# Optimization experiments

Hardware: AMD Instinct MI355X
Metric: run time of the kernel (lower is better)

## Reference

```python
import jax, jax.numpy as jnp
import numpy as np

B, N, R, S, FIN, NCLS, KNN = 16, 2048, 64, 64, 6, 40, 40


def _knn_laplacian(x, k):
    # pairwise squared distance -> gaussian affinity -> row-wise top-k sparsify
    # -> symmetric-normalized Laplacian  L = I - D^{-1/2} A D^{-1/2}
    xx = jnp.sum(x * x, axis=-1)                      # [B,N]
    inner = jnp.einsum('bnd,bmd->bnm', x, x)          # [B,N,N]
    dist = xx[:, :, None] + xx[:, None, :] - 2.0 * inner
    A = jnp.exp(-dist)
    kth = jax.lax.top_k(A, k)[0][..., -1]             # k-th largest per row [B,N]
    A = jnp.where(A >= kth[..., None], A, jnp.zeros((), A.dtype))
    d = jnp.sum(A, axis=-1)
    dis = jnp.where(d > 0, jax.lax.rsqrt(jnp.maximum(d, 1e-12)), jnp.zeros((), A.dtype))
    L = jnp.eye(A.shape[-1], dtype=A.dtype) - dis[:, :, None] * A * dis[:, None, :]
    return L


def _cheb_conv(x, L, w, b):
    # DenseChebConv, K=3: T0=x, T1=Lx, T2=2LT1-T0, then linear on concat
    t0 = x
    t1 = jnp.matmul(L, x)
    t2 = 2.0 * jnp.matmul(L, t1) - t0
    xc = jnp.concatenate([t0, t1, t2], axis=-1)       # [B,N,3*Fin]
    return jnp.matmul(xc, w) + b


def setup_inputs() -> dict:
    key = jax.random.key(0)
    ks = jax.random.split(key, 16)
    p = lambda k_, sh: (jax.random.normal(k_, sh, dtype=jnp.float32) * 0.02)
    return {
        'x': jax.random.normal(ks[0], (B, N, FIN), dtype=jnp.float32),
        'laplacian_Reeb': jax.random.normal(ks[1], (B, R, R), dtype=jnp.float32),
        'sccs': jax.random.randint(ks[2], (B, R, S), 0, N),
        'vertices_reeb': jax.random.normal(ks[3], (B * R, 3), dtype=jnp.float32),
        'edges_reeb': jax.random.randint(ks[4], (B, 128, 2), 0, R),
        'labels': jax.random.randint(ks[5], (B,), 0, NCLS),
        'k': KNN, 'batch_size': B, 'num_points': N,
        'conv1_w': p(ks[6], (3 * FIN, 128)), 'conv1_b': jnp.zeros((128,), jnp.float32),
        'conv2_w': p(ks[7], (3 * 128, 512)), 'conv2_b': jnp.zeros((512,), jnp.float32),
        'convReeb_w': p(ks[8], (3 * 128, 512)), 'convReeb_b': jnp.zeros((512,), jnp.float32),
        'fc1_w': p(ks[9], (1024, 512)), 'fc1_b': jnp.zeros((512,), jnp.float32),
        'fc2_w': p(ks[10], (512, 128)), 'fc2_b': jnp.zeros((128,), jnp.float32),
        'fc3_w': p(ks[11], (128, NCLS)), 'fc3_b': jnp.zeros((NCLS,), jnp.float32),
    }


def reference(x, laplacian_Reeb, sccs, vertices_reeb, edges_reeb, labels, k,
              batch_size, num_points, conv1_w, conv1_b, conv2_w, conv2_b,
              convReeb_w, convReeb_b, fc1_w, fc1_b, fc2_w, fc2_b, fc3_w, fc3_b):
    regs = []
    # graph build is under no_grad in the original
    L = jax.lax.stop_gradient(_knn_laplacian(x, k))
    out = jax.nn.relu(_cheb_conv(x, L, conv1_w, conv1_b))           # [B,N,128]
    regs.append(jnp.linalg.norm(jnp.einsum('bnf,bnm,bmg->bfg', out, L, out)) ** 2)

    # Reeb ragged segment-max pool (no_grad in original): gather SCC index
    # groups per Reeb node and max-reduce -> [B,R,128]
    gathered = jax.vmap(lambda o, s: o[s])(out, sccs)               # [B,R,S,128]
    Vertices_final_Reeb = jax.lax.stop_gradient(jnp.max(gathered, axis=2))
    laplacian_Reeb_final = jax.lax.stop_gradient(laplacian_Reeb)

    L2 = jax.lax.stop_gradient(_knn_laplacian(out, k))
    out = jax.nn.relu(_cheb_conv(out, L2, conv2_w, conv2_b))        # [B,N,512]
    regs.append(jnp.linalg.norm(jnp.einsum('bnf,bnm,bmg->bfg', out, L2, out)) ** 2)

    out_Reeb = jax.nn.relu(_cheb_conv(Vertices_final_Reeb, laplacian_Reeb_final,
                                      convReeb_w, convReeb_b))      # [B,R,512]
    regs.append(jnp.linalg.norm(jnp.einsum('brf,brq,bqg->bfg', out_Reeb,
                                           laplacian_Reeb_final, out_Reeb)) ** 2)

    out = jnp.max(out, axis=1)            # [B,512]
    out_Reeb = jnp.max(out_Reeb, axis=1)  # [B,512]
    out = jnp.concatenate([out_Reeb, out], axis=1)                  # [B,1024]

    out = jnp.matmul(out, fc1_w) + fc1_b
    regs.append(jnp.linalg.norm(fc1_w[:, 0]) ** 2); regs.append(fc1_b[0] ** 2)
    out = jax.nn.relu(out)
    out = jnp.matmul(out, fc2_w) + fc2_b
    regs.append(jnp.linalg.norm(fc2_w[:, 0]) ** 2); regs.append(fc2_b[0] ** 2)
    out = jax.nn.relu(out)
    out = jnp.matmul(out, fc3_w) + fc3_b
    regs.append(jnp.linalg.norm(fc3_w[:, 0]) ** 2); regs.append(fc3_b[0] ** 2)
    return out, jnp.stack(regs)
```

## Files before the change

kernel.cpp:

```cpp
#include <hip/hip_runtime.h>

#define NB 16
#define NP 2048
#define NR 64
#define NS 64
#define KSEL 40

typedef __attribute__((ext_vector_type(8))) short bf16x8;
typedef __attribute__((ext_vector_type(4))) float f32x4;

constexpr long aOUT1 = 0;
constexpr long aT1A  = aOUT1 + 16L*2048*128;
constexpr long aT2A  = aT1A  + 16L*2048*6;
constexpr long aZ1   = aT2A  + 16L*2048*6;
constexpr long aM1   = aZ1   + 16L*2048*128;
constexpr long aVALS1= aM1   + 16L*128*128;
constexpr long aDIS1 = aVALS1+ 16L*2048*64;
constexpr long aVALS2= aDIS1 + 16L*2048;
constexpr long aDIS2 = aVALS2+ 16L*2048*64;
constexpr long aXX2  = aDIS2 + 16L*2048;
constexpr long aXX1  = aXX2  + 16L*2048;
constexpr long aG4   = aXX1  + 16L*2048;
constexpr long aT1B  = aG4   + 4L*2048*2048;
constexpr long aT2B  = aT1B  + 16L*2048*128;
constexpr long aOUT2 = aT2B  + 16L*2048*128;
constexpr long aZ2   = aOUT2 + 16L*2048*512;
constexpr long aVFR  = aZ2   + 16L*2048*512;
constexpr long aT1R  = aVFR  + 16L*64*128;
constexpr long aT2R  = aT1R  + 16L*64*128;
constexpr long aOUTR = aT2R  + 16L*64*128;
constexpr long aZR   = aOUTR + 16L*64*512;
constexpr long aPOOL = aZR   + 16L*64*512;
constexpr long aFC1O = aPOOL + 16L*1024;
constexpr long aFC2O = aFC1O + 16L*512;
constexpr long aMPP  = aFC2O + 16L*128;
constexpr long FTOT  = aMPP  + 16L*8*512;

constexpr long iCOLS1 = 0;
constexpr long iCNT1  = iCOLS1 + 16L*2048*64;
constexpr long iCOLS2 = iCNT1  + 16L*2048;
constexpr long iCNT2  = iCOLS2 + 16L*2048*64;
constexpr long ITOT   = iCNT2  + 16L*2048;

constexpr long uOUT1H = 0;
constexpr long uOUT1L = uOUT1H + 16L*2048*128;
constexpr long uOUT1R = uOUT1L + 16L*2048*128;
constexpr long uT1BH  = uOUT1R + 16L*2048*128;
constexpr long uT1BL  = uT1BH  + 16L*2048*128;
constexpr long uT2BH  = uT1BL  + 16L*2048*128;
constexpr long uT2BL  = uT2BH  + 16L*2048*128;
constexpr long uW2TH  = uT2BL  + 16L*2048*128;
constexpr long uW2TL  = uW2TH  + 512L*384;
constexpr long uVFRH  = uW2TL  + 512L*384;
constexpr long uVFRL  = uVFRH  + 16L*64*128;
constexpr long uT1RH  = uVFRL  + 16L*64*128;
constexpr long uT1RL  = uT1RH  + 16L*64*128;
constexpr long uT2RH  = uT1RL  + 16L*64*128;
constexpr long uT2RL  = uT2RH  + 16L*64*128;
constexpr long uWRTH  = uT2RL  + 16L*64*128;
constexpr long uWRTL  = uWRTH  + 512L*384;
constexpr long uOUT1T = uWRTL  + 512L*384;
constexpr long uZ1T   = uOUT1T + 16L*128*2048;
constexpr long uOUT2T = uZ1T   + 16L*128*2048;
constexpr long uZ2T   = uOUT2T + 16L*512*2048;
constexpr long uOUTRT = uZ2T   + 16L*512*2048;
constexpr long uZRT   = uOUTRT + 16L*512*64;
constexpr long uOUT2B = uZRT   + 16L*512*64;
constexpr long UTOT   = uOUT2B + 16L*2048*512;

__device__ __align__(256) float  g_farena[FTOT];
__device__ __align__(256) int    g_iarena[ITOT];
__device__ __align__(256) ushort g_uarena[UTOT];

__device__ __forceinline__ float wsum_f(float v){
  #pragma unroll
  for (int s=32;s>0;s>>=1) v += __shfl_xor(v, s, 64);
  return v;
}
__device__ __forceinline__ int wsum_i(int v){
  #pragma unroll
  for (int s=32;s>0;s>>=1) v += __shfl_xor(v, s, 64);
  return v;
}

__device__ __forceinline__ void gl2lds16(const void* g, void* l){
  __builtin_amdgcn_global_load_lds(
      (const __attribute__((address_space(1))) void*)g,
      (__attribute__((address_space(3))) void*)l, 16, 0, 0);
}

__device__ __forceinline__ ushort bf_rne(float x){
  unsigned u = __float_as_uint(x);
  u += 0x7fffu + ((u >> 16) & 1u);
  return (ushort)(u >> 16);
}
__device__ __forceinline__ void bf_hilo(float x, ushort& h, ushort& l){
  unsigned u = __float_as_uint(x);
  h = (ushort)(u >> 16);
  float hf = __uint_as_float(u & 0xffff0000u);
  l = (ushort)(__float_as_uint(x - hf) >> 16);
}

__device__ __forceinline__ unsigned fkey(float f){
  unsigned b = __float_as_uint(f);
  return b ^ (((unsigned)((int)b >> 31)) | 0x80000000u);
}
__device__ __forceinline__ float fkey_inv(unsigned k){
  unsigned m = ((unsigned)((int)(~k) >> 31)) | 0x80000000u;
  return __uint_as_float(k ^ m);
}

__device__ __forceinline__ void topk_store(unsigned (&uk)[32], int lane, long row,
    int* __restrict__ cols, float* __restrict__ vals,
    int* __restrict__ cnt, float* __restrict__ dis)
{
  unsigned kmax = uk[0], kmin = uk[0];
  #pragma unroll
  for (int q=1;q<32;++q){
    kmax = kmax > uk[q] ? kmax : uk[q];
    kmin = kmin < uk[q] ? kmin : uk[q];
  }
  #pragma unroll
  for (int s=32;s>0;s>>=1){
    unsigned o1 = (unsigned)__shfl_xor((int)kmax, s, 64);
    unsigned o2 = (unsigned)__shfl_xor((int)kmin, s, 64);
    kmax = kmax > o1 ? kmax : o1;
    kmin = kmin < o2 ? kmin : o2;
  }
  unsigned lo = kmin, hi = kmax + 1u;
  int cLo = 2048, cHi = 0, it = 0;
  while (cLo != KSEL && hi - lo > 1u){
    unsigned t;
    if (it & 1){
      t = lo + ((hi - lo) >> 1);
    } else {
      float flo = fkey_inv(lo), fhi = fkey_inv(hi);
      float ft = flo + (fhi - flo) * ((float)(cLo - KSEL) / (float)(cLo - cHi));
      t = fkey(ft);
      if (t <= lo) t = lo + 1u;
      else if (t >= hi) t = hi - 1u;
    }
    ++it;
    int c = 0;
    #pragma unroll
    for (int q=0;q<32;++q) c += (int)__popcll(__ballot(uk[q] >= t));
    if (c >= KSEL){ lo = t; cLo = c; } else { hi = t; cHi = c; }
  }
  unsigned kth = lo;
  int kc = 0;
  #pragma unroll
  for (int q=0;q<32;++q) kc += (uk[q] >= kth) ? 1 : 0;
  int tot = wsum_i(kc);
  int incl = kc;
  #pragma unroll
  for (int s=1;s<64;s<<=1){ int u = __shfl_up(incl, s, 64); if (lane >= s) incl += u; }
  int pos = incl - kc;
  int* cp = cols + row*64; float* vp = vals + row*64;
  float d = 0.f;
  #pragma unroll
  for (int q=0;q<32;++q){
    if (uk[q] >= kth){
      float v = __expf(fkey_inv(uk[q]));
      d += v;
      if (pos < 64){ cp[pos] = q*64 + lane; vp[pos] = v; }
      pos++;
    }
  }
  d = wsum_f(d);
  if (lane == 0){
    cnt[row] = tot <= 64 ? tot : 64;
    dis[row] = d > 0.f ? (1.0f / sqrtf(fmaxf(d, 1e-12f))) : 0.f;
  }
}

__global__ __launch_bounds__(256) void xx6_kernel(const float* __restrict__ x,
    float* __restrict__ xx1)
{
  long i = (long)blockIdx.x*256 + threadIdx.x;
  const float* p = x + i*6;
  float2 v0 = *(const float2*)(p);
  float2 v1 = *(const float2*)(p+2);
  float2 v2 = *(const float2*)(p+4);
  xx1[i] = v0.x*v0.x + v0.y*v0.y + v1.x*v1.x + v1.y*v1.y + v2.x*v2.x + v2.y*v2.y;
}

__global__ __launch_bounds__(256) void knn1_kernel(const float* __restrict__ x,
    const float* __restrict__ xx1,
    int* __restrict__ cols, float* __restrict__ vals, int* __restrict__ cnt,
    float* __restrict__ dis)
{
  int lane = threadIdx.x & 63;
  long row = (long)blockIdx.x*4 + (threadIdx.x >> 6);
  int b = (int)(row >> 11); int i = (int)(row & (NP-1));
  const float* xb = x + (long)b*NP*6;
  const float* xxb = xx1 + ((long)b << 11);
  float xi[6];
  #pragma unroll
  for (int d2=0; d2<6; ++d2) xi[d2] = xb[(long)i*6 + d2];
  float xxi = xxb[i];
  unsigned uk[32];
  #pragma unroll 4
  for (int c=0;c<32;++c){
    int j = c*64 + lane;
    const float* xj = xb + (long)j*6;
    float2 v0 = *(const float2*)(xj);
    float2 v1 = *(const float2*)(xj+2);
    float2 v2 = *(const float2*)(xj+4);
    float inr = xi[0]*v0.x + xi[1]*v0.y + xi[2]*v1.x + xi[3]*v1.y + xi[4]*v2.x + xi[5]*v2.y;
    uk[c] = fkey(2.f*inr - xxi - xxb[j]);
  }
  topk_store(uk, lane, row, cols, vals, cnt, dis);
}

__global__ __launch_bounds__(256) void knn2_kernel(const float* __restrict__ G,
    const float* __restrict__ xx, int batch0,
    int* __restrict__ cols, float* __restrict__ vals, int* __restrict__ cnt,
    float* __restrict__ dis)
{
  int lane = threadIdx.x & 63;
  long lrow = (long)blockIdx.x*4 + (threadIdx.x >> 6);
  int lb = (int)(lrow >> 11); int i = (int)(lrow & (NP-1));
  long row = ((long)(batch0+lb) << 11) + i;
  const float* Gr = G + ((long)lb*NP + i)*NP;
  const float* xxb = xx + ((long)(batch0+lb) << 11);
  float xxi = xxb[i];
  unsigned uk[32];
  #pragma unroll 4
  for (int c=0;c<32;++c){
    int j = c*64 + lane;
    uk[c] = fkey(2.f*Gr[j] - xxi - xxb[j]);
  }
  topk_store(uk, lane, row, cols, vals, cnt, dis);
}

__global__ __launch_bounds__(256) void spmm6_kernel(const float* __restrict__ X,
    const float* __restrict__ T0, float* __restrict__ Y,
    const int* __restrict__ cols, const float* __restrict__ vals,
    const int* __restrict__ cnt, const float* __restrict__ dis,
    float c1, float c2, float cs)
{
  long row = (long)blockIdx.x*256 + threadIdx.x;
  int b = (int)(row >> 11);
  const float* Xb = X + ((long)b << 11)*6;
  const float* db = dis + ((long)b << 11);
  float acc[6] = {0,0,0,0,0,0};
  int c = cnt[row];
  const int* cp = cols + row*64; const float* vp = vals + row*64;
  for (int t=0;t<c;++t){
    int j = cp[t];
    float w = vp[t] * db[j];
    const float* xr = Xb + (long)j*6;
    #pragma unroll
    for (int d2=0; d2<6; ++d2) acc[d2] += w * xr[d2];
  }
  float di = dis[row];
  #pragma unroll
  for (int d2=0; d2<6; ++d2)
    Y[row*6+d2] = c1*X[row*6+d2] + c2*T0[row*6+d2] - cs*di*acc[d2];
}

template<int W, bool PACK>
__global__ __launch_bounds__((W >= 256) ? 256 : W) void spmm_kernel(
    const float* __restrict__ X, const float* __restrict__ T0, float* __restrict__ Y,
    ushort* __restrict__ Hh, ushort* __restrict__ Ll,
    const int* __restrict__ cols, const float* __restrict__ vals,
    const int* __restrict__ cnt, const float* __restrict__ dis,
    float c1, float c2, float cs)
{
  constexpr int TPB = (W >= 256) ? 256 : W;
  constexpr int E = W / TPB;
  __shared__ int scol[64];
  __shared__ float sval[64];
  int q = blockIdx.x;
  long row = ((long)(q & 7) << 12) + (q >> 3);
  int b = (int)(row >> 11);
  int tid = threadIdx.x;
  int c = cnt[row];
  if (tid < 64){ scol[tid] = cols[row*64+tid]; sval[tid] = vals[row*64+tid]; }
  __syncthreads();
  const float* Xb = X + ((long)b << 11)*W;
  const float* db = dis + ((long)b << 11);
  float acc[E] = {};
  for (int t=0;t<c;++t){
    int j = scol[t];
    float w = sval[t] * db[j];
    const float* xr = Xb + (long)j*W;
    #pragma unroll
    for (int e=0;e<E;++e) acc[e] += w * xr[tid + e*TPB];
  }
  float di = dis[row];
  #pragma unroll
  for (int e=0;e<E;++e){
    long idx = row*W + tid + e*TPB;
    float y = c1*X[idx] + c2*T0[idx] - cs*di*acc[e];
    Y[idx] = y;
    if (PACK){
      ushort h, l; bf_hilo(y, h, l);
      Hh[idx] = h; Ll[idx] = l;
    }
  }
}

__global__ __launch_bounds__(256) void spmmb_kernel(
    const float* __restrict__ X, const ushort* __restrict__ Xb,
    float* __restrict__ Y,
    const int* __restrict__ cols, const float* __restrict__ vals,
    const int* __restrict__ cnt, const float* __restrict__ dis)
{
  __shared__ int scol[4][64];
  __shared__ float sval[4][64];
  int q = blockIdx.x;
  int wid = threadIdx.x >> 6, lane = threadIdx.x & 63;
  long row = ((long)(q & 7) << 12) + ((long)(q >> 3) << 2) + wid;
  int b = (int)(row >> 11);
  scol[wid][lane] = cols[row*64 + lane];
  sval[wid][lane] = vals[row*64 + lane];
  const ushort* Xbb = Xb + ((long)b << 11)*512;
  const float* db = dis + ((long)b << 11);
  int c = cnt[row];
  float acc[8] = {};
  for (int t=0;t<c;++t){
    int j = scol[wid][t];
    float w = sval[wid][t] * db[j];
    bf16x8 v = *(const bf16x8*)(Xbb + (long)j*512 + lane*8);
    #pragma unroll
    for (int e=0;e<8;++e)
      acc[e] += w * __uint_as_float(((unsigned)(ushort)v[e]) << 16);
  }
  float di = dis[row];
  long base = row*512 + lane*8;
  float4 x0 = *(const float4*)(X + base);
  float4 x1 = *(const float4*)(X + base + 4);
  float4 o0, o1;
  o0.x = x0.x - di*acc[0]; o0.y = x0.y - di*acc[1];
  o0.z = x0.z - di*acc[2]; o0.w = x0.w - di*acc[3];
  o1.x = x1.x - di*acc[4]; o1.y = x1.y - di*acc[5];
  o1.z = x1.z - di*acc[6]; o1.w = x1.w - di*acc[7];
  *(float4*)(Y + base) = o0;
  *(float4*)(Y + base + 4) = o1;
}

__global__ __launch_bounds__(128) void conv1_kernel(const float* __restrict__ x,
    const float* __restrict__ t1, const float* __restrict__ t2,
    const float* __restrict__ w, const float* __restrict__ bias,
    float* __restrict__ out, ushort* __restrict__ oh, ushort* __restrict__ ol,
    ushort* __restrict__ orr)
{
  long row = blockIdx.x; int o = threadIdx.x;
  float acc = bias[o];
  const float* xr = x + row*6; const float* a1 = t1 + row*6; const float* a2 = t2 + row*6;
  #pragma unroll
  for (int d2=0; d2<6; ++d2){
    acc += xr[d2]*w[d2*128 + o];
    acc += a1[d2]*w[(6+d2)*128 + o];
    acc += a2[d2]*w[(12+d2)*128 + o];
  }
  acc = fmaxf(acc, 0.f);
  long idx = row*128 + o;
  out[idx] = acc;
  ushort h, l; bf_hilo(acc, h, l);
  oh[idx] = h; ol[idx] = l;
  orr[idx] = bf_rne(acc);
}

template<bool HILO>
__global__ __launch_bounds__(256) void tpack_kernel(const float* __restrict__ X,
    ushort* __restrict__ H, ushort* __restrict__ L,
    int R, int C, long sIn, long sOut)
{
  __shared__ float tile[32][33];
  int c0 = blockIdx.x*32, r0 = blockIdx.y*32, b = blockIdx.z;
  const float* Xb = X + (long)b*sIn;
  int tx = threadIdx.x & 31, ty = threadIdx.x >> 5;
  #pragma unroll
  for (int rr=ty; rr<32; rr+=8)
    tile[rr][tx] = Xb[(long)(r0+rr)*C + c0+tx];
  __syncthreads();
  #pragma unroll
  for (int cc=ty; cc<32; cc+=8){
    float xv = tile[tx][cc];
    long oidx = (long)b*sOut + (long)(c0+cc)*R + r0 + tx;
    if (HILO){
      ushort h, l; bf_hilo(xv, h, l);
      H[oidx] = h; L[oidx] = l;
    } else {
      H[oidx] = bf_rne(xv);
    }
  }
}

template<bool SPLIT, bool CHEB, bool BR, bool TRI>
__global__ __launch_bounds__(256) void mgemm_kernel(
    const ushort* __restrict__ Ah0, const ushort* __restrict__ Ah1, const ushort* __restrict__ Ah2,
    const ushort* __restrict__ Al0, const ushort* __restrict__ Al1, const ushort* __restrict__ Al2,
    const ushort* __restrict__ Bh, const ushort* __restrict__ Bl,
    const float* __restrict__ bias, float* __restrict__ C,
    ushort* __restrict__ Cb, float* __restrict__ ssq,
    int M, int N, int K, long sA, long sB, long sC)
{
  __shared__ ushort AsH[128*32];
  __shared__ ushort BsH[128*32];
  __shared__ ushort AsL[SPLIT ? 128*32 : 8];
  __shared__ ushort BsL[SPLIT ? 128*32 : 8];
  int bz = blockIdx.z;
  int m0, n0;
  if constexpr (TRI){
    int t = blockIdx.x, bx = 0, rem = 16;
    while (t >= rem){ t -= rem; --rem; ++bx; }
    m0 = bx*128; n0 = (bx + t)*128;
  } else {
    m0 = blockIdx.x*128; n0 = blockIdx.y*128;
  }
  int tid = threadIdx.x, lane = tid & 63, wid = tid >> 6;
  int wm = (wid & 1)*64, wn = (wid >> 1)*64;
  f32x4 acc[4][4] = {};
  const ushort* Bb  = Bh + (long)bz*sB;
  const ushort* Blb = SPLIT ? (Bl + (long)bz*sB) : (const ushort*)nullptr;
  const ushort* Ab  = CHEB ? Ah0 : (Ah0 + (long)bz*sA);
  const ushort* Alb = (SPLIT && !CHEB) ? (Al0 + (long)bz*sA) : Al0;

  for (int k0 = 0; k0 < K; k0 += 32){
    #pragma unroll
    for (int cc2=0; cc2<2; ++cc2){
      int chunk = wid*2 + cc2;
      int e = chunk*512 + lane*8;
      int row = e >> 5;
      int slot = (e >> 3) & 3;
      int scol = (slot ^ ((row >> 1) & 3)) * 8;
      const ushort* asrc;
      if (CHEB){
        int kg2 = k0 + scol;
        const ushort* base = (kg2 < 128) ? Ah0 : ((kg2 < 256) ? Ah1 : Ah2);
        asrc = base + (long)(m0+row)*128 + (kg2 & 127);
      } else {
        asrc = Ab + (long)(m0+row)*K + k0 + scol;
      }
      gl2lds16(asrc, &AsH[chunk*512]);
      gl2lds16(Bb + (long)(n0+row)*K + k0 + scol, &BsH[chunk*512]);
      if (SPLIT){
        const ushort* alsrc;
        if (CHEB){
          int kg2 = k0 + scol;
          const ushort* base = (kg2 < 128) ? Al0 : ((kg2 < 256) ? Al1 : Al2);
          alsrc = base + (long)(m0+row)*128 + (kg2 & 127);
        } else {
          alsrc = Alb + (long)(m0+row)*K + k0 + scol;
        }
        gl2lds16(alsrc, &AsL[chunk*512]);
        gl2lds16(Blb + (long)(n0+row)*K + k0 + scol, &BsL[chunk*512]);
      }
    }
    __syncthreads();
    int lr = lane & 15, kg = lane >> 4;
    bf16x8 af[4], bfr[4];
    #pragma unroll
    for (int f=0; f<4; ++f){
      int ra = wm + f*16 + lr;
      int rb = wn + f*16 + lr;
      af[f]  = *(const bf16x8*)&AsH[ra*32 + (kg ^ ((ra>>1)&3))*8];
      bfr[f] = *(const bf16x8*)&BsH[rb*32 + (kg ^ ((rb>>1)&3))*8];
    }
    if (SPLIT){
      bf16x8 al[4], bl[4];
      #pragma unroll
      for (int f=0; f<4; ++f){
        int ra = wm + f*16 + lr;
        int rb = wn + f*16 + lr;
        al[f] = *(const bf16x8*)&AsL[ra*32 + (kg ^ ((ra>>1)&3))*8];
        bl[f] = *(const bf16x8*)&BsL[rb*32 + (kg ^ ((rb>>1)&3))*8];
      }
      #pragma unroll
      for (int mf=0; mf<4; ++mf)
        #pragma unroll
        for (int nf=0; nf<4; ++nf){
          acc[mf][nf] = __builtin_amdgcn_mfma_f32_16x16x32_bf16(af[mf], bfr[nf], acc[mf][nf], 0,0,0);
          acc[mf][nf] = __builtin_amdgcn_mfma_f32_16x16x32_bf16(af[mf], bl[nf],  acc[mf][nf], 0,0,0);
          acc[mf][nf] = __builtin_amdgcn_mfma_f32_16x16x32_bf16(al[mf], bfr[nf], acc[mf][nf], 0,0,0);
        }
    } else {
      #pragma unroll
      for (int mf=0; mf<4; ++mf)
        #pragma unroll
        for (int nf=0; nf<4; ++nf)
          acc[mf][nf] = __builtin_amdgcn_mfma_f32_16x16x32_bf16(af[mf], bfr[nf], acc[mf][nf], 0,0,0);
    }
    __syncthreads();
  }
  int lr = lane & 15, l4 = (lane >> 4)*4;
  if (ssq){
    float s = 0.f;
    #pragma unroll
    for (int mf=0; mf<4; ++mf)
      #pragma unroll
      for (int nf=0; nf<4; ++nf)
        #pragma unroll
        for (int r=0; r<4; ++r){ float v = acc[mf][nf][r]; s += v*v; }
    s = wsum_f(s);
    if (lane == 0) atomicAdd(ssq, s);
    return;
  }
  #pragma unroll
  for (int mf=0; mf<4; ++mf){
    #pragma unroll
    for (int nf=0; nf<4; ++nf){
      int n = n0 + wn + nf*16 + lr;
      float bv = BR ? bias[n] : 0.f;
      #pragma unroll
      for (int r=0; r<4; ++r){
        int m = m0 + wm + mf*16 + l4 + r;
        float v = acc[mf][nf][r];
        if (BR) v = fmaxf(v + bv, 0.f);
        C[(long)bz*sC + (long)m*N + n] = v;
        if (TRI) C[(long)bz*sC + (long)n*N + m] = v;
        if (Cb) Cb[(long)bz*sC + (long)m*N + n] = bf_rne(v);
      }
    }
  }
}

__global__ __launch_bounds__(256) void rownorm_kernel(const float* __restrict__ X,
    float* __restrict__ xx)
{
  int lane = threadIdx.x & 63;
  long row = (long)blockIdx.x*4 + (threadIdx.x >> 6);
  const float* p = X + row*128;
  float v0 = p[lane], v1 = p[64+lane];
  float s = wsum_f(v0*v0 + v1*v1);
  if (lane == 0) xx[row] = s;
}

__global__ __launch_bounds__(128) void reeb_pool_kernel(const float* __restrict__ out1,
    const int* __restrict__ sccs, float* __restrict__ VfR,
    ushort* __restrict__ Hh, ushort* __restrict__ Ll)
{
  int q = blockIdx.x;
  int br = ((q & 7) << 7) + (q >> 3);
  int b = br >> 6;
  int f = threadIdx.x;
  const int* sp = sccs + (long)br*NS;
  const float* ob = out1 + ((long)b << 11)*128;
  float m = -1e30f;
  for (int s=0;s<NS;++s){
    int idx = sp[s];
    m = fmaxf(m, ob[(long)idx*128 + f]);
  }
  long oidx = (long)br*128 + f;
  VfR[oidx] = m;
  ushort h, l; bf_hilo(m, h, l);
  Hh[oidx] = h; Ll[oidx] = l;
}

template<int W, bool PACK>
__global__ __launch_bounds__((W>=256)?256:W) void reeb_mm_kernel(const float* __restrict__ Lap,
    const float* __restrict__ X, const float* __restrict__ T0, float* __restrict__ Y,
    ushort* __restrict__ Hh, ushort* __restrict__ Ll,
    float cs, float c2)
{
  constexpr int TPB = (W>=256)?256:W;
  constexpr int E = W/TPB;
  int br = blockIdx.x; int b = br >> 6; int r = br & 63;
  const float* lr = Lap + ((long)b*NR + r)*NR;
  const float* Xb = X + (long)b*NR*W;
  int tid = threadIdx.x;
  float acc[E] = {};
  for (int q=0;q<NR;++q){
    float w = lr[q];
    #pragma unroll
    for (int e=0;e<E;++e) acc[e] += w * Xb[(long)q*W + tid + e*TPB];
  }
  #pragma unroll
  for (int e=0;e<E;++e){
    long idx = (long)br*W + tid + e*TPB;
    float y = cs*acc[e] + c2*T0[idx];
    Y[idx] = y;
    if (PACK){
      ushort h, l; bf_hilo(y, h, l);
      Hh[idx] = h; Ll[idx] = l;
    }
  }
}

__global__ __launch_bounds__(512) void maxpool1_kernel(const float* __restrict__ X,
    float* __restrict__ part)
{
  int b = blockIdx.x, rc = blockIdx.y; int f = threadIdx.x;
  const float* p = X + ((long)b*2048 + (long)rc*256)*512 + f;
  float m = -1e30f;
  #pragma unroll 4
  for (int r=0;r<256;++r) m = fmaxf(m, p[(long)r*512]);
  part[((long)b*8+rc)*512 + f] = m;
}

__global__ __launch_bounds__(512) void maxpool2_kernel(const float* __restrict__ part,
    const float* __restrict__ outR, float* __restrict__ pool)
{
  int b = blockIdx.x; int f = threadIdx.x;
  const float* pp = part + (long)b*8*512 + f;
  float m = -1e30f;
  #pragma unroll
  for (int r=0;r<8;++r) m = fmaxf(m, pp[r*512]);
  pool[(long)b*1024 + 512 + f] = m;
  const float* rp = outR + (long)b*64*512 + f;
  float mr = -1e30f;
  #pragma unroll 4
  for (int r=0;r<64;++r) mr = fmaxf(mr, rp[(long)r*512]);
  pool[(long)b*1024 + f] = mr;
}

template<bool RELU>
__global__ __launch_bounds__(256) void fc_kernel(const float* __restrict__ in,
    const float* __restrict__ W, const float* __restrict__ bias,
    float* __restrict__ out, int IN, int OUT)
{
  __shared__ float red[4][64];
  int b = blockIdx.x, o0 = blockIdx.y*64;
  int tid = threadIdx.x;
  int ol = tid & 63, q = tid >> 6;
  int o = o0 + ol;
  const float* ip = in + (long)b*IN;
  float acc = 0.f;
  if (o < OUT){
    int kb = IN >> 2;
    int ks = q*kb;
    for (int i=0;i<kb;i+=8){
      #pragma unroll
      for (int u=0;u<8;++u){
        int k = ks + i + u;
        acc += ip[k]*W[(long)k*OUT + o];
      }
    }
  }
  red[q][ol] = acc;
  __syncthreads();
  if (tid < 64){
    int oo = o0 + tid;
    if (oo < OUT){
      float s = red[0][tid]+red[1][tid]+red[2][tid]+red[3][tid] + bias[oo];
      out[(long)b*OUT + oo] = RELU ? fmaxf(s, 0.f) : s;
    }
  }
}

__global__ __launch_bounds__(256) void wreg_kernel(const float* __restrict__ w1,
    const float* __restrict__ b1, const float* __restrict__ w2, const float* __restrict__ b2,
    const float* __restrict__ w3, const float* __restrict__ b3, float* __restrict__ out9)
{
  __shared__ float ps[3][4];
  int tid = threadIdx.x, lane = tid & 63, wid = tid >> 6;
  float s1 = 0.f, s2 = 0.f, s3 = 0.f;
  for (int i=tid;i<1024;i+=256){ float v = w1[(long)i*512]; s1 += v*v; }
  for (int i=tid;i<512;i+=256){ float v = w2[(long)i*128]; s2 += v*v; }
  if (tid < 128){ float v = w3[(long)tid*40]; s3 = v*v; }
  s1 = wsum_f(s1); s2 = wsum_f(s2); s3 = wsum_f(s3);
  if (lane == 0){ ps[0][wid]=s1; ps[1][wid]=s2; ps[2][wid]=s3; }
  __syncthreads();
  if (tid == 0){
    out9[3] = ps[0][0]+ps[0][1]+ps[0][2]+ps[0][3];
    out9[4] = b1[0]*b1[0];
    out9[5] = ps[1][0]+ps[1][1]+ps[1][2]+ps[1][3];
    out9[6] = b2[0]*b2[0];
    out9[7] = ps[2][0]+ps[2][1]+ps[2][2]+ps[2][3];
    out9[8] = b3[0]*b3[0];
  }
}

extern "C" void kernel_launch(void* const* d_in, const int* in_sizes, int n_in,
                              void* d_out, int out_size, void* d_ws, size_t ws_size,
                              hipStream_t stream)
{
  (void)in_sizes; (void)n_in; (void)d_ws; (void)ws_size; (void)out_size;
  const float* x    = (const float*)d_in[0];
  const float* lapR = (const float*)d_in[1];
  const int*   sccs = (const int*)d_in[2];
  const float* w1   = (const float*)d_in[9];
  const float* b1   = (const float*)d_in[10];
  const float* w2   = (const float*)d_in[11];
  const float* b2   = (const float*)d_in[12];
  const float* wR   = (const float*)d_in[13];
  const float* bRb  = (const float*)d_in[14];
  const float* fw1  = (const float*)d_in[15];
  const float* fb1  = (const float*)d_in[16];
  const float* fw2  = (const float*)d_in[17];
  const float* fb2  = (const float*)d_in[18];
  const float* fw3  = (const float*)d_in[19];
  const float* fb3  = (const float*)d_in[20];
  float* out = (float*)d_out;

  float* Fb = nullptr; int* Ib = nullptr; ushort* Ub = nullptr;
  hipGetSymbolAddress((void**)&Fb, HIP_SYMBOL(g_farena));
  hipGetSymbolAddress((void**)&Ib, HIP_SYMBOL(g_iarena));
  hipGetSymbolAddress((void**)&Ub, HIP_SYMBOL(g_uarena));

  float* out1 = Fb + aOUT1;  float* t1a = Fb + aT1A;  float* t2a = Fb + aT2A;
  float* Z1   = Fb + aZ1;    float* M1  = Fb + aM1;
  float* vals1= Fb + aVALS1; float* dis1= Fb + aDIS1;
  float* vals2= Fb + aVALS2; float* dis2= Fb + aDIS2;
  float* xx2  = Fb + aXX2;   float* xx1 = Fb + aXX1;  float* G4  = Fb + aG4;
  float* t1b  = Fb + aT1B;   float* t2b = Fb + aT2B;
  float* out2 = Fb + aOUT2;  float* Z2  = Fb + aZ2;
  float* VfR  = Fb + aVFR;   float* t1R = Fb + aT1R;  float* t2R= Fb + aT2R;
  float* outR = Fb + aOUTR;  float* ZR  = Fb + aZR;
  float* pool = Fb + aPOOL;  float* fc1o= Fb + aFC1O; float* fc2o=Fb + aFC2O;
  float* mpp  = Fb + aMPP;
  (void)M1;
  int* cols1 = Ib + iCOLS1; int* cnt1 = Ib + iCNT1;
  int* cols2 = Ib + iCOLS2; int* cnt2 = Ib + iCNT2;
  ushort* out1h = Ub + uOUT1H; ushort* out1l = Ub + uOUT1L;
  ushort* out1r = Ub + uOUT1R;
  ushort* t1bh  = Ub + uT1BH;  ushort* t1bl  = Ub + uT1BL;
  ushort* t2bh  = Ub + uT2BH;  ushort* t2bl  = Ub + uT2BL;
  ushort* w2th  = Ub + uW2TH;  ushort* w2tl  = Ub + uW2TL;
  ushort* vfrh  = Ub + uVFRH;  ushort* vfrl  = Ub + uVFRL;
  ushort* t1rh  = Ub + uT1RH;  ushort* t1rl  = Ub + uT1RL;
  ushort* t2rh  = Ub + uT2RH;  ushort* t2rl  = Ub + uT2RL;
  ushort* wrth  = Ub + uWRTH;  ushort* wrtl  = Ub + uWRTL;
  ushort* out1t = Ub + uOUT1T; ushort* z1t   = Ub + uZ1T;
  ushort* out2t = Ub + uOUT2T; ushort* z2t   = Ub + uZ2T;
  ushort* outrt = Ub + uOUTRT; ushort* zrt   = Ub + uZRT;
  ushort* out2b = Ub + uOUT2B;

  hipMemsetAsync(out + 640, 0, 9*sizeof(float), stream);

  xx6_kernel<<<dim3(128),dim3(256),0,stream>>>(x, xx1);
  knn1_kernel<<<dim3(8192),dim3(256),0,stream>>>(x, xx1, cols1, vals1, cnt1, dis1);
  spmm6_kernel<<<dim3(128),dim3(256),0,stream>>>(x, x, t1a, cols1, vals1, cnt1, dis1, 1.f, 0.f, 1.f);
  spmm6_kernel<<<dim3(128),dim3(256),0,stream>>>(t1a, x, t2a, cols1, vals1, cnt1, dis1, 2.f, -1.f, 2.f);
  conv1_kernel<<<dim3(32768),dim3(128),0,stream>>>(x, t1a, t2a, w1, b1, out1, out1h, out1l, out1r);

  spmm_kernel<128,false><<<dim3(32768),dim3(128),0,stream>>>(out1, out1, Z1, nullptr, nullptr,
      cols1, vals1, cnt1, dis1, 1.f, 0.f, 1.f);
  tpack_kernel<false><<<dim3(4,64,16),dim3(256),0,stream>>>(out1, out1t, nullptr, 2048,128, 2048L*128, 128L*2048);
  tpack_kernel<false><<<dim3(4,64,16),dim3(256),0,stream>>>(Z1,   z1t,   nullptr, 2048,128, 2048L*128, 128L*2048);
  mgemm_kernel<false,false,false,false><<<dim3(1,1,16),dim3(256),0,stream>>>(
      out1t,nullptr,nullptr, nullptr,nullptr,nullptr, z1t,nullptr, nullptr, nullptr,
      nullptr, out+640, 128,128,2048, 128L*2048, 128L*2048, 0);
  reeb_pool_kernel<<<dim3(1024),dim3(128),0,stream>>>(out1, sccs, VfR, vfrh, vfrl);

  rownorm_kernel<<<dim3(8192),dim3(256),0,stream>>>(out1, xx2);
  for (int g=0; g<4; ++g){
    long off = (long)g*4*NP*128;
    mgemm_kernel<false,false,false,true><<<dim3(136,1,4),dim3(256),0,stream>>>(
        out1r+off,nullptr,nullptr, nullptr,nullptr,nullptr, out1r+off, nullptr, nullptr, G4,
        nullptr, nullptr, 2048,2048,128, (long)NP*128, (long)NP*128, (long)NP*NP);
    knn2_kernel<<<dim3(2048),dim3(256),0,stream>>>(G4, xx2, g*4, cols2, vals2, cnt2, dis2);
  }
  spmm_kernel<128,true><<<dim3(32768),dim3(128),0,stream>>>(out1, out1, t1b, t1bh, t1bl,
      cols2, vals2, cnt2, dis2, 1.f, 0.f, 1.f);
  spmm_kernel<128,true><<<dim3(32768),dim3(128),0,stream>>>(t1b, out1, t2b, t2bh, t2bl,
      cols2, vals2, cnt2, dis2, 2.f, -1.f, 2.f);
  tpack_kernel<true><<<dim3(16,12,1),dim3(256),0,stream>>>(w2, w2th, w2tl, 384,512, 0,0);
  mgemm_kernel<true,true,true,false><<<dim3(256,4,1),dim3(256),0,stream>>>(
      out1h,t1bh,t2bh, out1l,t1bl,t2bl, w2th, w2tl, b2, out2,
      out2b, nullptr, 32768,512,384, 0,0,0);
  spmmb_kernel<<<dim3(8192),dim3(256),0,stream>>>(out2, out2b, Z2, cols2, vals2, cnt2, dis2);
  tpack_kernel<false><<<dim3(16,64,16),dim3(256),0,stream>>>(out2, out2t, nullptr, 2048,512, 2048L*512, 512L*2048);
  tpack_kernel<false><<<dim3(16,64,16),dim3(256),0,stream>>>(Z2,   z2t,   nullptr, 2048,512, 2048L*512, 512L*2048);
  mgemm_kernel<false,false,false,false><<<dim3(4,4,16),dim3(256),0,stream>>>(
      out2t,nullptr,nullptr, nullptr,nullptr,nullptr, z2t,nullptr, nullptr, nullptr,
      nullptr, out+641, 512,512,2048, 512L*2048, 512L*2048, 0);

  reeb_mm_kernel<128,true><<<dim3(1024),dim3(128),0,stream>>>(lapR, VfR, VfR, t1R, t1rh, t1rl, 1.f, 0.f);
  reeb_mm_kernel<128,true><<<dim3(1024),dim3(128),0,stream>>>(lapR, t1R, VfR, t2R, t2rh, t2rl, 2.f, -1.f);
  tpack_kernel<true><<<dim3(16,12,1),dim3(256),0,stream>>>(wR, wrth, wrtl, 384,512, 0,0);
  mgemm_kernel<true,true,true,false><<<dim3(8,4,1),dim3(256),0,stream>>>(
      vfrh,t1rh,t2rh, vfrl,t1rl,t2rl, wrth, wrtl, bRb, outR,
      nullptr, nullptr, 1024,512,384, 0,0,0);
  reeb_mm_kernel<512,false><<<dim3(1024),dim3(256),0,stream>>>(lapR, outR, outR, ZR, nullptr, nullptr, 1.f, 0.f);
  tpack_kernel<false><<<dim3(16,2,16),dim3(256),0,stream>>>(outR, outrt, nullptr, 64,512, 64L*512, 512L*64);
  tpack_kernel<false><<<dim3(16,2,16),dim3(256),0,stream>>>(ZR,   zrt,   nullptr, 64,512, 64L*512, 512L*64);
  mgemm_kernel<false,false,false,false><<<dim3(4,4,16),dim3(256),0,stream>>>(
      outrt,nullptr,nullptr, nullptr,nullptr,nullptr, zrt,nullptr, nullptr, nullptr,
      nullptr, out+642, 512,512,64, 512L*64, 512L*64, 0);

  maxpool1_kernel<<<dim3(16,8),dim3(512),0,stream>>>(out2, mpp);
  maxpool2_kernel<<<dim3(16),dim3(512),0,stream>>>(mpp, outR, pool);
  fc_kernel<true ><<<dim3(16,8),dim3(256),0,stream>>>(pool, fw1, fb1, fc1o, 1024, 512);
  fc_kernel<true ><<<dim3(16,2),dim3(256),0,stream>>>(fc1o, fw2, fb2, fc2o, 512, 128);
  fc_kernel<false><<<dim3(16,1),dim3(256),0,stream>>>(fc2o, fw3, fb3, out, 128, 40);
  wreg_kernel<<<dim3(1),dim3(256),0,stream>>>(fw1, fb1, fw2, fb2, fw3, fb3, out+640);
}
```

Measured before the change: 1.207 ms.

## Drop weight low-part split, compute full Gram in one launch, float-distance top-k

The conv2 and Reeb weight GEMMs now use a single bf16 copy of the weights, dropping one of three MFMA passes and the low-part weight loads. The four batched triangular Gram GEMM launches plus per-group knn2 launches are replaced by one full 16x16x16 grid GEMM into a buffer sized for all batches, followed by one knn2 launch. The top-k selection now searches on clamped non-negative squared distances directly instead of order-preserving integer keys, with an early exit when the minimum value alone covers k entries. These changes cut MFMA work, LDS traffic and launch count, at the cost of lower weight precision, computing the symmetric Gram twice, and a much larger scratch buffer.

```diff
diff --git a/kernel.cpp b/kernel.cpp
--- a/kernel.cpp
+++ b/kernel.cpp
@@ -13,15 +13,14 @@
 constexpr long aT1A  = aOUT1 + 16L*2048*128;
 constexpr long aT2A  = aT1A  + 16L*2048*6;
 constexpr long aZ1   = aT2A  + 16L*2048*6;
-constexpr long aM1   = aZ1   + 16L*2048*128;
-constexpr long aVALS1= aM1   + 16L*128*128;
+constexpr long aVALS1= aZ1   + 16L*2048*128;
 constexpr long aDIS1 = aVALS1+ 16L*2048*64;
 constexpr long aVALS2= aDIS1 + 16L*2048;
 constexpr long aDIS2 = aVALS2+ 16L*2048*64;
 constexpr long aXX2  = aDIS2 + 16L*2048;
 constexpr long aXX1  = aXX2  + 16L*2048;
-constexpr long aG4   = aXX1  + 16L*2048;
-constexpr long aT1B  = aG4   + 4L*2048*2048;
+constexpr long aG    = aXX1  + 16L*2048;
+constexpr long aT1B  = aG    + 16L*2048*2048;
 constexpr long aT2B  = aT1B  + 16L*2048*128;
 constexpr long aOUT2 = aT2B  + 16L*2048*128;
 constexpr long aZ2   = aOUT2 + 16L*2048*512;
@@ -49,17 +48,15 @@
 constexpr long uT1BL  = uT1BH  + 16L*2048*128;
 constexpr long uT2BH  = uT1BL  + 16L*2048*128;
 constexpr long uT2BL  = uT2BH  + 16L*2048*128;
-constexpr long uW2TH  = uT2BL  + 16L*2048*128;
-constexpr long uW2TL  = uW2TH  + 512L*384;
-constexpr long uVFRH  = uW2TL  + 512L*384;
+constexpr long uW2T   = uT2BL  + 16L*2048*128;
+constexpr long uVFRH  = uW2T   + 512L*384;
 constexpr long uVFRL  = uVFRH  + 16L*64*128;
 constexpr long uT1RH  = uVFRL  + 16L*64*128;
 constexpr long uT1RL  = uT1RH  + 16L*64*128;
 constexpr long uT2RH  = uT1RL  + 16L*64*128;
 constexpr long uT2RL  = uT2RH  + 16L*64*128;
-constexpr long uWRTH  = uT2RL  + 16L*64*128;
-constexpr long uWRTL  = uWRTH  + 512L*384;
-constexpr long uOUT1T = uWRTL  + 512L*384;
+constexpr long uWRT   = uT2RL  + 16L*64*128;
+constexpr long uOUT1T = uWRT   + 512L*384;
 constexpr long uZ1T   = uOUT1T + 16L*128*2048;
 constexpr long uOUT2T = uZ1T   + 16L*128*2048;
 constexpr long uZ2T   = uOUT2T + 16L*512*2048;
@@ -101,55 +98,50 @@
   l = (ushort)(__float_as_uint(x - hf) >> 16);
 }
 
-__device__ __forceinline__ unsigned fkey(float f){
-  unsigned b = __float_as_uint(f);
-  return b ^ (((unsigned)((int)b >> 31)) | 0x80000000u);
-}
-__device__ __forceinline__ float fkey_inv(unsigned k){
-  unsigned m = ((unsigned)((int)(~k) >> 31)) | 0x80000000u;
-  return __uint_as_float(k ^ m);
-}
-
-__device__ __forceinline__ void topk_store(unsigned (&uk)[32], int lane, long row,
+__device__ __forceinline__ void topk_store(float (&dk)[32], int lane, long row,
     int* __restrict__ cols, float* __restrict__ vals,
     int* __restrict__ cnt, float* __restrict__ dis)
 {
-  unsigned kmax = uk[0], kmin = uk[0];
-  #pragma unroll
-  for (int q=1;q<32;++q){
-    kmax = kmax > uk[q] ? kmax : uk[q];
-    kmin = kmin < uk[q] ? kmin : uk[q];
-  }
+  float dmin = dk[0], dmax = dk[0];
+  #pragma unroll
+  for (int q=1;q<32;++q){ dmin = fminf(dmin, dk[q]); dmax = fmaxf(dmax, dk[q]); }
   #pragma unroll
   for (int s=32;s>0;s>>=1){
-    unsigned o1 = (unsigned)__shfl_xor((int)kmax, s, 64);
-    unsigned o2 = (unsigned)__shfl_xor((int)kmin, s, 64);
-    kmax = kmax > o1 ? kmax : o1;
-    kmin = kmin < o2 ? kmin : o2;
-  }
-  unsigned lo = kmin, hi = kmax + 1u;
-  int cLo = 2048, cHi = 0, it = 0;
-  while (cLo != KSEL && hi - lo > 1u){
-    unsigned t;
-    if (it & 1){
-      t = lo + ((hi - lo) >> 1);
-    } else {
-      float flo = fkey_inv(lo), fhi = fkey_inv(hi);
-      float ft = flo + (fhi - flo) * ((float)(cLo - KSEL) / (float)(cLo - cHi));
-      t = fkey(ft);
-      if (t <= lo) t = lo + 1u;
-      else if (t >= hi) t = hi - 1u;
-    }
-    ++it;
-    int c = 0;
-    #pragma unroll
-    for (int q=0;q<32;++q) c += (int)__popcll(__ballot(uk[q] >= t));
-    if (c >= KSEL){ lo = t; cLo = c; } else { hi = t; cHi = c; }
-  }
-  unsigned kth = lo;
+    dmin = fminf(dmin, __shfl_xor(dmin, s, 64));
+    dmax = fmaxf(dmax, __shfl_xor(dmax, s, 64));
+  }
+  int c0 = 0;
+  #pragma unroll
+  for (int q=0;q<32;++q) c0 += (int)__popcll(__ballot(dk[q] <= dmin));
+  float kth;
+  if (c0 >= KSEL){
+    kth = dmin;
+  } else {
+    float lo = dmin, hi = dmax;
+    int cLo = c0, cHi = 2048, it = 0;
+    while (cHi != KSEL && __float_as_uint(hi) - __float_as_uint(lo) > 1u){
+      float t;
+      if (it & 1){
+        t = __uint_as_float((__float_as_uint(lo) + __float_as_uint(hi)) >> 1);
+      } else {
+        t = lo + (hi - lo) * ((float)(KSEL - cLo) / (float)(cHi - cLo));
+        unsigned tb = __float_as_uint(t);
+        unsigned lb = __float_as_uint(lo), hb = __float_as_uint(hi);
+        if (tb <= lb) tb = lb + 1u;
+        else if (tb >= hb) tb = hb - 1u;
+        t = __uint_as_float(tb);
+      }
+      ++it;
+      int c = 0;
+      #pragma unroll
+      for (int q=0;q<32;++q) c += (int)__popcll(__ballot(dk[q] <= t));
+      if (c >= KSEL){ hi = t; cHi = c; } else { lo = t; cLo = c; }
+    }
+    kth = hi;
+  }
   int kc = 0;
   #pragma unroll
-  for (int q=0;q<32;++q) kc += (uk[q] >= kth) ? 1 : 0;
+  for (int q=0;q<32;++q) kc += (dk[q] <= kth) ? 1 : 0;
   int tot = wsum_i(kc);
   int incl = kc;
   #pragma unroll
@@ -159,8 +151,8 @@
   float d = 0.f;
   #pragma unroll
   for (int q=0;q<32;++q){
-    if (uk[q] >= kth){
-      float v = __expf(fkey_inv(uk[q]));
+    if (dk[q] <= kth){
+      float v = __expf(-dk[q]);
       d += v;
       if (pos < 64){ cp[pos] = q*64 + lane; vp[pos] = v; }
       pos++;
@@ -198,7 +190,7 @@
   #pragma unroll
   for (int d2=0; d2<6; ++d2) xi[d2] = xb[(long)i*6 + d2];
   float xxi = xxb[i];
-  unsigned uk[32];
+  float dk[32];
   #pragma unroll 4
   for (int c=0;c<32;++c){
     int j = c*64 + lane;
@@ -207,30 +199,29 @@
     float2 v1 = *(const float2*)(xj+2);
     float2 v2 = *(const float2*)(xj+4);
     float inr = xi[0]*v0.x + xi[1]*v0.y + xi[2]*v1.x + xi[3]*v1.y + xi[4]*v2.x + xi[5]*v2.y;
-    uk[c] = fkey(2.f*inr - xxi - xxb[j]);
-  }
-  topk_store(uk, lane, row, cols, vals, cnt, dis);
+    dk[c] = fmaxf(xxi + xxb[j] - 2.f*inr, 0.f);
+  }
+  topk_store(dk, lane, row, cols, vals, cnt, dis);
 }
 
 __global__ __launch_bounds__(256) void knn2_kernel(const float* __restrict__ G,
-    const float* __restrict__ xx, int batch0,
+    const float* __restrict__ xx,
     int* __restrict__ cols, float* __restrict__ vals, int* __restrict__ cnt,
     float* __restrict__ dis)
 {
   int lane = threadIdx.x & 63;
-  long lrow = (long)blockIdx.x*4 + (threadIdx.x >> 6);
-  int lb = (int)(lrow >> 11); int i = (int)(lrow & (NP-1));
-  long row = ((long)(batch0+lb) << 11) + i;
-  const float* Gr = G + ((long)lb*NP + i)*NP;
-  const float* xxb = xx + ((long)(batch0+lb) << 11);
+  long row = (long)blockIdx.x*4 + (threadIdx.x >> 6);
+  const float* Gr = G + row*NP;
+  const float* xxb = xx + ((row >> 11) << 11);
+  int i = (int)(row & (NP-1));
   float xxi = xxb[i];
-  unsigned uk[32];
+  float dk[32];
   #pragma unroll 4
   for (int c=0;c<32;++c){
     int j = c*64 + lane;
-    uk[c] = fkey(2.f*Gr[j] - xxi - xxb[j]);
-  }
-  topk_store(uk, lane, row, cols, vals, cnt, dis);
+    dk[c] = fmaxf(xxi + xxb[j] - 2.f*Gr[j], 0.f);
+  }
+  topk_store(dk, lane, row, cols, vals, cnt, dis);
 }
 
 __global__ __launch_bounds__(256) void spmm6_kernel(const float* __restrict__ X,
@@ -389,35 +380,26 @@
   }
 }
 
-template<bool SPLIT, bool CHEB, bool BR, bool TRI>
+template<bool SPLITA, bool CHEB, bool BR>
 __global__ __launch_bounds__(256) void mgemm_kernel(
     const ushort* __restrict__ Ah0, const ushort* __restrict__ Ah1, const ushort* __restrict__ Ah2,
     const ushort* __restrict__ Al0, const ushort* __restrict__ Al1, const ushort* __restrict__ Al2,
-    const ushort* __restrict__ Bh, const ushort* __restrict__ Bl,
+    const ushort* __restrict__ Bh,
     const float* __restrict__ bias, float* __restrict__ C,
     ushort* __restrict__ Cb, float* __restrict__ ssq,
     int M, int N, int K, long sA, long sB, long sC)
 {
   __shared__ ushort AsH[128*32];
   __shared__ ushort BsH[128*32];
-  __shared__ ushort AsL[SPLIT ? 128*32 : 8];
-  __shared__ ushort BsL[SPLIT ? 128*32 : 8];
+  __shared__ ushort AsL[SPLITA ? 128*32 : 8];
   int bz = blockIdx.z;
-  int m0, n0;
-  if constexpr (TRI){
-    int t = blockIdx.x, bx = 0, rem = 16;
-    while (t >= rem){ t -= rem; --rem; ++bx; }
-    m0 = bx*128; n0 = (bx + t)*128;
-  } else {
-    m0 = blockIdx.x*128; n0 = blockIdx.y*128;
-  }
+  int m0 = blockIdx.x*128, n0 = blockIdx.y*128;
   int tid = threadIdx.x, lane = tid & 63, wid = tid >> 6;
   int wm = (wid & 1)*64, wn = (wid >> 1)*64;
   f32x4 acc[4][4] = {};
-  const ushort* Bb  = Bh + (long)bz*sB;
-  const ushort* Blb = SPLIT ? (Bl + (long)bz*sB) : (const ushort*)nullptr;
-  const ushort* Ab  = CHEB ? Ah0 : (Ah0 + (long)bz*sA);
-  const ushort* Alb = (SPLIT && !CHEB) ? (Al0 + (long)bz*sA) : Al0;
+  const ushort* Bb = Bh + (long)bz*sB;
+  const ushort* Ab = CHEB ? Ah0 : (Ah0 + (long)bz*sA);
+  const ushort* Alb = (SPLITA && !CHEB) ? (Al0 + (long)bz*sA) : Al0;
 
   for (int k0 = 0; k0 < K; k0 += 32){
     #pragma unroll
@@ -437,7 +419,7 @@
       }
       gl2lds16(asrc, &AsH[chunk*512]);
       gl2lds16(Bb + (long)(n0+row)*K + k0 + scol, &BsH[chunk*512]);
-      if (SPLIT){
+      if (SPLITA){
         const ushort* alsrc;
         if (CHEB){
           int kg2 = k0 + scol;
@@ -447,7 +429,6 @@
           alsrc = Alb + (long)(m0+row)*K + k0 + scol;
         }
         gl2lds16(alsrc, &AsL[chunk*512]);
-        gl2lds16(Blb + (long)(n0+row)*K + k0 + scol, &BsL[chunk*512]);
       }
     }
     __syncthreads();
@@ -460,21 +441,18 @@
       af[f]  = *(const bf16x8*)&AsH[ra*32 + (kg ^ ((ra>>1)&3))*8];
       bfr[f] = *(const bf16x8*)&BsH[rb*32 + (kg ^ ((rb>>1)&3))*8];
     }
-    if (SPLIT){
-      bf16x8 al[4], bl[4];
+    if (SPLITA){
+      bf16x8 al[4];
       #pragma unroll
       for (int f=0; f<4; ++f){
         int ra = wm + f*16 + lr;
-        int rb = wn + f*16 + lr;
         al[f] = *(const bf16x8*)&AsL[ra*32 + (kg ^ ((ra>>1)&3))*8];
-        bl[f] = *(const bf16x8*)&BsL[rb*32 + (kg ^ ((rb>>1)&3))*8];
       }
       #pragma unroll
       for (int mf=0; mf<4; ++mf)
         #pragma unroll
         for (int nf=0; nf<4; ++nf){
           acc[mf][nf] = __builtin_amdgcn_mfma_f32_16x16x32_bf16(af[mf], bfr[nf], acc[mf][nf], 0,0,0);
-          acc[mf][nf] = __builtin_amdgcn_mfma_f32_16x16x32_bf16(af[mf], bl[nf],  acc[mf][nf], 0,0,0);
           acc[mf][nf] = __builtin_amdgcn_mfma_f32_16x16x32_bf16(al[mf], bfr[nf], acc[mf][nf], 0,0,0);
         }
     } else {
@@ -511,7 +489,6 @@
         float v = acc[mf][nf][r];
         if (BR) v = fmaxf(v + bv, 0.f);
         C[(long)bz*sC + (long)m*N + n] = v;
-        if (TRI) C[(long)bz*sC + (long)n*N + m] = v;
         if (Cb) Cb[(long)bz*sC + (long)m*N + n] = bf_rne(v);
       }
     }
@@ -692,28 +669,27 @@
   hipGetSymbolAddress((void**)&Ub, HIP_SYMBOL(g_uarena));
 
   float* out1 = Fb + aOUT1;  float* t1a = Fb + aT1A;  float* t2a = Fb + aT2A;
-  float* Z1   = Fb + aZ1;    float* M1  = Fb + aM1;
+  float* Z1   = Fb + aZ1;
   float* vals1= Fb + aVALS1; float* dis1= Fb + aDIS1;
   float* vals2= Fb + aVALS2; float* dis2= Fb + aDIS2;
-  float* xx2  = Fb + aXX2;   float* xx1 = Fb + aXX1;  float* G4  = Fb + aG4;
+  float* xx2  = Fb + aXX2;   float* xx1 = Fb + aXX1;  float* G  = Fb + aG;
   float* t1b  = Fb + aT1B;   float* t2b = Fb + aT2B;
   float* out2 = Fb + aOUT2;  float* Z2  = Fb + aZ2;
   float* VfR  = Fb + aVFR;   float* t1R = Fb + aT1R;  float* t2R= Fb + aT2R;
   float* outR = Fb + aOUTR;  float* ZR  = Fb + aZR;
   float* pool = Fb + aPOOL;  float* fc1o= Fb + aFC1O; float* fc2o=Fb + aFC2O;
   float* mpp  = Fb + aMPP;
-  (void)M1;
   int* cols1 = Ib + iCOLS1; int* cnt1 = Ib + iCNT1;
   int* cols2 = Ib + iCOLS2; int* cnt2 = Ib + iCNT2;
   ushort* out1h = Ub + uOUT1H; ushort* out1l = Ub + uOUT1L;
   ushort* out1r = Ub + uOUT1R;
   ushort* t1bh  = Ub + uT1BH;  ushort* t1bl  = Ub + uT1BL;
   ushort* t2bh  = Ub + uT2BH;  ushort* t2bl  = Ub + uT2BL;
-  ushort* w2th  = Ub + uW2TH;  ushort* w2tl  = Ub + uW2TL;
+  ushort* w2t   = Ub + uW2T;
   ushort* vfrh  = Ub + uVFRH;  ushort* vfrl  = Ub + uVFRL;
   ushort* t1rh  = Ub + uT1RH;  ushort* t1rl  = Ub + uT1RL;
   ushort* t2rh  = Ub + uT2RH;  ushort* t2rl  = Ub + uT2RL;
-  ushort* wrth  = Ub + uWRTH;  ushort* wrtl  = Ub + uWRTL;
+  ushort* wrt   = Ub + uWRT;
   ushort* out1t = Ub + uOUT1T; ushort* z1t   = Ub + uZ1T;
   ushort* out2t = Ub + uOUT2T; ushort* z2t   = Ub + uZ2T;
   ushort* outrt = Ub + uOUTRT; ushort* zrt   = Ub + uZRT;
@@ -731,45 +707,43 @@
       cols1, vals1, cnt1, dis1, 1.f, 0.f, 1.f);
   tpack_kernel<false><<<dim3(4,64,16),dim3(256),0,stream>>>(out1, out1t, nullptr, 2048,128, 2048L*128, 128L*2048);
   tpack_kernel<false><<<dim3(4,64,16),dim3(256),0,stream>>>(Z1,   z1t,   nullptr, 2048,128, 2048L*128, 128L*2048);
-  mgemm_kernel<false,false,false,false><<<dim3(1,1,16),dim3(256),0,stream>>>(
-      out1t,nullptr,nullptr, nullptr,nullptr,nullptr, z1t,nullptr, nullptr, nullptr,
+  mgemm_kernel<false,false,false><<<dim3(1,1,16),dim3(256),0,stream>>>(
+      out1t,nullptr,nullptr, nullptr,nullptr,nullptr, z1t, nullptr, nullptr,
       nullptr, out+640, 128,128,2048, 128L*2048, 128L*2048, 0);
   reeb_pool_kernel<<<dim3(1024),dim3(128),0,stream>>>(out1, sccs, VfR, vfrh, vfrl);
 
   rownorm_kernel<<<dim3(8192),dim3(256),0,stream>>>(out1, xx2);
-  for (int g=0; g<4; ++g){
-    long off = (long)g*4*NP*128;
-    mgemm_kernel<false,false,false,true><<<dim3(136,1,4),dim3(256),0,stream>>>(
-        out1r+off,nullptr,nullptr, nullptr,nullptr,nullptr, out1r+off, nullptr, nullptr, G4,
-        nullptr, nullptr, 2048,2048,128, (long)NP*128, (long)NP*128, (long)NP*NP);
-    knn2_kernel<<<dim3(2048),dim3(256),0,stream>>>(G4, xx2, g*4, cols2, vals2, cnt2, dis2);
-  }
+  mgemm_kernel<false,false,false><<<dim3(16,16,16),dim3(256),0,stream>>>(
+      out1r,nullptr,nullptr, nullptr,nullptr,nullptr, out1r, nullptr, G,
+      nullptr, nullptr, 2048,2048,128, (long)NP*128, (long)NP*128, (long)NP*NP);
+  knn2_kernel<<<dim3(8192),dim3(256),0,stream>>>(G, xx2, cols2, vals2, cnt2, dis2);
+
   spmm_kernel<128,true><<<dim3(32768),dim3(128),0,stream>>>(out1, out1, t1b, t1bh, t1bl,
       cols2, vals2, cnt2, dis2, 1.f, 0.f, 1.f);
   spmm_kernel<128,true><<<dim3(32768),dim3(128),0,stream>>>(t1b, out1, t2b, t2bh, t2bl,
       cols2, vals2, cnt2, dis2, 2.f, -1.f, 2.f);
-  tpack_kernel<true><<<dim3(16,12,1),dim3(256),0,stream>>>(w2, w2th, w2tl, 384,512, 0,0);
-  mgemm_kernel<true,true,true,false><<<dim3(256,4,1),dim3(256),0,stream>>>(
-      out1h,t1bh,t2bh, out1l,t1bl,t2bl, w2th, w2tl, b2, out2,
+  tpack_kernel<false><<<dim3(16,12,1),dim3(256),0,stream>>>(w2, w2t, nullptr, 384,512, 0,0);
+  mgemm_kernel<true,true,true><<<dim3(256,4,1),dim3(256),0,stream>>>(
+      out1h,t1bh,t2bh, out1l,t1bl,t2bl, w2t, b2, out2,
       out2b, nullptr, 32768,512,384, 0,0,0);
   spmmb_kernel<<<dim3(8192),dim3(256),0,stream>>>(out2, out2b, Z2, cols2, vals2, cnt2, dis2);
   tpack_kernel<false><<<dim3(16,64,16),dim3(256),0,stream>>>(out2, out2t, nullptr, 2048,512, 2048L*512, 512L*2048);
   tpack_kernel<false><<<dim3(16,64,16),dim3(256),0,stream>>>(Z2,   z2t,   nullptr, 2048,512, 2048L*512, 512L*2048);
-  mgemm_kernel<false,false,false,false><<<dim3(4,4,16),dim3(256),0,stream>>>(
-      out2t,nullptr,nullptr, nullptr,nullptr,nullptr, z2t,nullptr, nullptr, nullptr,
+  mgemm_kernel<false,false,false><<<dim3(4,4,16),dim3(256),0,stream>>>(
+      out2t,nullptr,nullptr, nullptr,nullptr,nullptr, z2t, nullptr, nullptr,
       nullptr, out+641, 512,512,2048, 512L*2048, 512L*2048, 0);
 
   reeb_mm_kernel<128,true><<<dim3(1024),dim3(128),0,stream>>>(lapR, VfR, VfR, t1R, t1rh, t1rl, 1.f, 0.f);
   reeb_mm_kernel<128,true><<<dim3(1024),dim3(128),0,stream>>>(lapR, t1R, VfR, t2R, t2rh, t2rl, 2.f, -1.f);
-  tpack_kernel<true><<<dim3(16,12,1),dim3(256),0,stream>>>(wR, wrth, wrtl, 384,512, 0,0);
-  mgemm_kernel<true,true,true,false><<<dim3(8,4,1),dim3(256),0,stream>>>(
-      vfrh,t1rh,t2rh, vfrl,t1rl,t2rl, wrth, wrtl, bRb, outR,
+  tpack_kernel<false><<<dim3(16,12,1),dim3(256),0,stream>>>(wR, wrt, nullptr, 384,512, 0,0);
+  mgemm_kernel<true,true,true><<<dim3(8,4,1),dim3(256),0,stream>>>(
+      vfrh,t1rh,t2rh, vfrl,t1rl,t2rl, wrt, bRb, outR,
       nullptr, nullptr, 1024,512,384, 0,0,0);
   reeb_mm_kernel<512,false><<<dim3(1024),dim3(256),0,stream>>>(lapR, outR, outR, ZR, nullptr, nullptr, 1.f, 0.f);
   tpack_kernel<false><<<dim3(16,2,16),dim3(256),0,stream>>>(outR, outrt, nullptr, 64,512, 64L*512, 512L*64);
   tpack_kernel<false><<<dim3(16,2,16),dim3(256),0,stream>>>(ZR,   zrt,   nullptr, 64,512, 64L*512, 512L*64);
-  mgemm_kernel<false,false,false,false><<<dim3(4,4,16),dim3(256),0,stream>>>(
-      outrt,nullptr,nullptr, nullptr,nullptr,nullptr, zrt,nullptr, nullptr, nullptr,
+  mgemm_kernel<false,false,false><<<dim3(4,4,16),dim3(256),0,stream>>>(
+      outrt,nullptr,nullptr, nullptr,nullptr,nullptr, zrt, nullptr, nullptr,
       nullptr, out+642, 512,512,64, 512L*64, 512L*64, 0);
 
   maxpool1_kernel<<<dim3(16,8),dim3(512),0,stream>>>(out2, mpp);
```

Result: faster. 1.098 ms (-9.0%).
